# Kernel tuning notes

Measured on AMD Instinct MI355X. Metric: run time of the kernel, lower is better.

The kernel has to match this reference:

```python
import jax, jax.numpy as jnp
import numpy as np

# dims
B, N = 8, 16384
MODEL_DIM = 256
F = 32        # feature_dim
H = 4         # num_heads
G = 32        # grid_size
G3 = G * G * G
EPS = 1e-5


def setup_inputs() -> dict:
    key = jax.random.key(0)
    ks = jax.random.split(key, 9)
    eye = jnp.broadcast_to(jnp.eye(3, dtype=jnp.float32), (H, 3, 3))
    return {
        "input_tensor": jax.random.normal(ks[0], (B, MODEL_DIM, N), dtype=jnp.float32),
        "original_points": jax.random.normal(ks[1], (B, 3, N), dtype=jnp.float32),
        # Conv1d kernel_size=1, no bias -> plain (out,in) matmul weight
        "W_kv": jax.random.normal(ks[2], (H * (F + 3), MODEL_DIM), dtype=jnp.float32) * 0.02,
        # key BN affine (orig init weight=0; use small random to exercise path)
        "key_gamma": jax.random.normal(ks[3], (H * 3,), dtype=jnp.float32) * 0.1,
        "key_beta": jax.random.normal(ks[4], (H * 3,), dtype=jnp.float32) * 0.1,
        "val_gamma": 1.0 + jax.random.normal(ks[5], (H * F,), dtype=jnp.float32) * 0.1,
        "val_beta": jax.random.normal(ks[6], (H * F,), dtype=jnp.float32) * 0.1,
        # VolTransformer: per-head affine (rotation-ish matrix + translation)
        "R": eye + jax.random.normal(ks[7], (H, 3, 3), dtype=jnp.float32) * 0.05,
        "t": jax.random.normal(ks[8], (H, 3), dtype=jnp.float32) * 0.1,
    }


def _bn(x, gamma, beta):
    # training-mode BatchNorm1d over (batch, length) per channel; x: (B, C, N)
    mean = jnp.mean(x, axis=(0, 2), keepdims=True)
    var = jnp.var(x, axis=(0, 2), keepdims=True)
    xhat = (x - mean) * jax.lax.rsqrt(var + EPS)
    return xhat * gamma[None, :, None] + beta[None, :, None]


def reference(input_tensor, original_points, W_kv, key_gamma, key_beta,
              val_gamma, val_beta, R, t):
    # 1x1 conv == channel matmul: (B, H*(F+3), N)
    kv = jnp.einsum('om,bmn->bon', W_kv, input_tensor)
    keys_offset = _bn(kv[:, :H * 3], key_gamma, key_beta)          # (B, H*3, N)
    values = _bn(kv[:, H * 3:], val_gamma, val_beta)               # (B, H*F, N)

    keys_offset = keys_offset.reshape(B, H, 3, N)
    pts = original_points[:, None, :, :] + keys_offset             # (B,H,3,N)
    # per-head affine transform (VolTransformer)
    tk = jnp.einsum('hij,bhjn->bhin', R, pts) + t[None, :, :, None]
    lattice = jnp.tanh(tk)                                         # in (-1,1)

    # DifferentiablePositions: map (-1,1) -> [0, G-1], lower corner + local frac
    pos = (lattice + 1.0) * (0.5 * (G - 1))                        # (B,H,3,N)
    idx0 = jnp.clip(jnp.floor(pos), 0.0, G - 2).astype(jnp.int32)  # (B,H,3,N)
    local = pos - idx0                                             # (B,H,3,N)

    values_t = values.reshape(B, H, F, N).transpose(0, 1, 3, 2)    # (B,H,N,F)
    bh_off = (jnp.arange(B * H, dtype=jnp.int32).reshape(B, H) * G3)[:, :, None]

    out = jnp.zeros((B * H * G3, F), dtype=values.dtype)
    # trilinear splat-scatter over the 8 grid corners
    for cx in (0, 1):
        wx = local[:, :, 0] if cx else 1.0 - local[:, :, 0]
        for cy in (0, 1):
            wy = local[:, :, 1] if cy else 1.0 - local[:, :, 1]
            for cz in (0, 1):
                wz = local[:, :, 2] if cz else 1.0 - local[:, :, 2]
                w = wx * wy * wz                                    # (B,H,N)
                flat = ((idx0[:, :, 0] + cx) * G + (idx0[:, :, 1] + cy)) * G \
                       + (idx0[:, :, 2] + cz)                       # (B,H,N)
                seg = (bh_off + flat).reshape(-1)                   # (B*H*N,)
                data = (values_t * w[..., None]).reshape(-1, F)
                out = out + jax.ops.segment_sum(data, seg, num_segments=B * H * G3)

    # (B, H*F, G, G, G)
    return out.reshape(B, H, G3, F).transpose(0, 1, 3, 2).reshape(B, H * F, G, G, G)
```

## Files before the change

### kernel.cpp

```cpp
#include <hip/hip_runtime.h>
#include <hip/hip_bf16.h>
#include <cstddef>

#define Bz 8
#define Nn 16384
#define MD 256
#define Ff 32
#define Hh 4
#define Gg 32
#define G3v 32768
#define CKV 140
#define NG 32
#define NBX 31
#define NBY 31
#define NBZ 31
#define NB2 953312
#define NCH 931

using bf16x8 = __attribute__((ext_vector_type(8))) short;
using f32x16 = __attribute__((ext_vector_type(16))) float;

__device__ __forceinline__ unsigned bf16rne(float f) {
    unsigned u = __float_as_uint(f);
    return (u + 0x7fffu + ((u >> 16) & 1u)) >> 16;
}
__device__ __forceinline__ unsigned cvt2(float lo, float hi) {
    __hip_bfloat162 hb = __float22bfloat162_rn(make_float2(lo, hi));
    union { __hip_bfloat162 b; unsigned u; } c;
    c.b = hb;
    return c.u;
}

__global__ __launch_bounds__(256) void prep_w_kernel(const float* __restrict__ W,
                                                     unsigned short* __restrict__ Wbf)
{
    const int idx = blockIdx.x * 256 + threadIdx.x;
    const int e    = idx & 7;
    const int rest = idx >> 3;
    const int m    = rest % 160;
    const int kg   = rest / 160;
    const int k    = (kg << 3) + e;
    Wbf[idx] = (m < CKV) ? (unsigned short)bf16rne(W[m * MD + k]) : (unsigned short)0;
}

__global__ __launch_bounds__(256, 3) void gemm_stats_kernel(
    const float* __restrict__ X, const unsigned short* __restrict__ Wbf,
    float* __restrict__ vals, float* __restrict__ keys,
    float* __restrict__ gsum, float* __restrict__ gsq)
{
    __shared__ unsigned XlU[4096];
    __shared__ unsigned WlU[5120];
    __shared__ float red[280];

    const int bid = blockIdx.x;
    const int b   = bid >> 7;
    const int n0  = (bid & 127) << 7;
    const int t   = threadIdx.x;
    const int w   = t >> 6;
    const int ln  = t & 31;
    const int hi  = (t >> 5) & 1;

    f32x16 acc[5];
    #pragma unroll
    for (int mt = 0; mt < 5; ++mt)
        #pragma unroll
        for (int j = 0; j < 16; ++j) acc[mt][j] = 0.f;

    for (int ks = 0; ks < 4; ++ks) {
        const int k0 = ks << 6;
        if (ks > 0) __syncthreads();

        #pragma unroll
        for (int it = 0; it < 4; ++it) {
            const int a  = t + (it << 8);
            const int kp = a >> 5;
            const int n4 = (a & 31) << 2;
            const float4 r0 = *reinterpret_cast<const float4*>(
                X + (size_t)(b * MD + k0 + 2 * kp) * Nn + n0 + n4);
            const float4 r1 = *reinterpret_cast<const float4*>(
                X + (size_t)(b * MD + k0 + 2 * kp + 1) * Nn + n0 + n4);
            const int base = ((kp >> 2) << 9) + (n4 << 2) + (kp & 3);
            XlU[base]      = cvt2(r0.x, r1.x);
            XlU[base + 4]  = cvt2(r0.y, r1.y);
            XlU[base + 8]  = cvt2(r0.z, r1.z);
            XlU[base + 12] = cvt2(r0.w, r1.w);
        }
        {
            const unsigned* src = reinterpret_cast<const unsigned*>(Wbf) + ks * 5120;
            #pragma unroll
            for (int i = 0; i < 5; ++i) {
                const int d4 = (t + (i << 8)) << 2;
                *reinterpret_cast<uint4*>(&WlU[d4]) =
                    *reinterpret_cast<const uint4*>(&src[d4]);
            }
        }
        __syncthreads();

        const short* xs = reinterpret_cast<const short*>(XlU);
        const short* ws = reinterpret_cast<const short*>(WlU);
        #pragma unroll
        for (int kk = 0; kk < 4; ++kk) {
            const int grp = (kk << 1) + hi;
            const bf16x8 bf = *reinterpret_cast<const bf16x8*>(
                xs + (((grp << 7) + (w << 5) + ln) << 3));
            #pragma unroll
            for (int mt = 0; mt < 5; ++mt) {
                const bf16x8 af = *reinterpret_cast<const bf16x8*>(
                    ws + ((grp * 160 + (mt << 5) + ln) << 3));
                acc[mt] = __builtin_amdgcn_mfma_f32_32x32x16_bf16(af, bf, acc[mt], 0, 0, 0);
            }
        }
    }

    const int n = n0 + (w << 5) + ln;
    #pragma unroll
    for (int mt = 0; mt < 5; ++mt)
        #pragma unroll
        for (int reg = 0; reg < 16; ++reg) {
            const int ml = (reg & 3) + ((reg >> 2) << 3) + (hi << 2);
            const int c  = mt * 32 + ml;
            const float v = acc[mt][reg];
            if (c < 12) {
                const int hh = c / 3, kk2 = c - (c / 3) * 3;
                keys[(size_t)((b * Hh + hh) * 3 + kk2) * Nn + n] = v;
            } else if (c < CKV) {
                const int cv = c - 12;
                vals[((size_t)(b * Hh + (cv >> 5)) * Nn + n) * Ff + (cv & 31)] = v;
            }
        }

    red[t] = 0.f;
    if (t < 24) red[256 + t] = 0.f;
    __syncthreads();
    #pragma unroll
    for (int mt = 0; mt < 5; ++mt)
        #pragma unroll
        for (int reg = 0; reg < 16; ++reg) {
            if (mt == 4 && reg >= 8) continue;
            const int ml = (reg & 3) + ((reg >> 2) << 3) + (hi << 2);
            const int c  = mt * 32 + ml;
            float s = acc[mt][reg];
            float q = s * s;
            #pragma unroll
            for (int off = 1; off < 32; off <<= 1) {
                s += __shfl_xor(s, off);
                q += __shfl_xor(q, off);
            }
            if (ln == 0 && c < CKV) {
                atomicAdd(&red[c], s);
                atomicAdd(&red[140 + c], q);
            }
        }
    __syncthreads();
    if (t < CKV) {
        atomicAdd(&gsum[t], red[t]);
        atomicAdd(&gsq[t],  red[140 + t]);
    }
}

__global__ void finalize_kernel(const float* __restrict__ gsum, const float* __restrict__ gsq,
                                const float* __restrict__ kg, const float* __restrict__ kb,
                                const float* __restrict__ vg, const float* __restrict__ vb,
                                float* __restrict__ scale, float* __restrict__ shift)
{
    const int c = threadIdx.x;
    if (c < CKV) {
        const float inv = 1.f / (float)(Bz * Nn);
        const float m = gsum[c] * inv;
        const float v = fmaf(-m, m, gsq[c] * inv);
        float ga, be;
        if (c < 12) { ga = kg[c]; be = kb[c]; }
        else        { ga = vg[c - 12]; be = vb[c - 12]; }
        const float sc = ga * rsqrtf(v + 1e-5f);
        scale[c] = sc;
        shift[c] = fmaf(-m, sc, be);
    }
}

__global__ __launch_bounds__(256) void points_kernel(
    const float* __restrict__ keys, const float* __restrict__ orig,
    const float* __restrict__ Rm, const float* __restrict__ tv,
    const float* __restrict__ scale, const float* __restrict__ shift,
    float4* __restrict__ rec, int* __restrict__ cnt)
{
    const int bid = blockIdx.x;
    const int g   = bid >> 6;
    const int b   = g >> 2;
    const int h   = g & 3;
    const int t   = threadIdx.x;
    const int n   = ((bid & 63) << 8) + t;

    __shared__ float sR[9], st3[3], ksc[3], ksh[3];
    if (t < 9)       sR[t] = Rm[h * 9 + t];
    else if (t < 12) st3[t - 9] = tv[h * 3 + (t - 9)];
    else if (t < 15) { ksc[t - 12] = scale[h * 3 + (t - 12)];
                       ksh[t - 12] = shift[h * 3 + (t - 12)]; }
    __syncthreads();

    const float k0 = fmaf(keys[(size_t)(g * 3 + 0) * Nn + n], ksc[0], ksh[0]);
    const float k1 = fmaf(keys[(size_t)(g * 3 + 1) * Nn + n], ksc[1], ksh[1]);
    const float k2 = fmaf(keys[(size_t)(g * 3 + 2) * Nn + n], ksc[2], ksh[2]);
    const float p0 = orig[(size_t)(b * 3 + 0) * Nn + n] + k0;
    const float p1 = orig[(size_t)(b * 3 + 1) * Nn + n] + k1;
    const float p2 = orig[(size_t)(b * 3 + 2) * Nn + n] + k2;

    int   idx[3];
    float loc[3];
    #pragma unroll
    for (int d = 0; d < 3; ++d) {
        const float tk = fmaf(sR[d*3+0], p0, fmaf(sR[d*3+1], p1, fmaf(sR[d*3+2], p2, st3[d])));
        const float la = tanhf(tk);
        const float po = (la + 1.f) * 15.5f;
        float fi = floorf(po);
        fi = fminf(fmaxf(fi, 0.f), 30.f);
        idx[d] = (int)fi;
        loc[d] = po - fi;
    }

    const unsigned meta = (unsigned)n | ((unsigned)idx[2] << 14) |
                          ((unsigned)idx[1] << 19) | ((unsigned)idx[0] << 24);
    float4 r;
    r.x = __uint_as_float(meta);
    r.y = loc[0]; r.z = loc[1]; r.w = loc[2];
    rec[(size_t)g * Nn + n] = r;
    const int key = ((g * NBX + idx[0]) * NBY + idx[1]) * NBZ + idx[2];
    atomicAdd(&cnt[key], 1);
}

__global__ __launch_bounds__(256) void scan1_kernel(const int* __restrict__ cnt,
                                                    int* __restrict__ bsum)
{
    __shared__ int s[256];
    const int t = threadIdx.x;
    const int i = blockIdx.x * 1024 + t * 4;
    int v = 0;
    #pragma unroll
    for (int j = 0; j < 4; ++j) { const int idx = i + j; if (idx < NB2) v += cnt[idx]; }
    s[t] = v;
    __syncthreads();
    for (int off = 128; off > 0; off >>= 1) {
        if (t < off) s[t] += s[t + off];
        __syncthreads();
    }
    if (t == 0) bsum[blockIdx.x] = s[0];
}

__global__ __launch_bounds__(1024) void scan2_kernel(const int* __restrict__ bsum,
                                                     int* __restrict__ bscan)
{
    __shared__ int s[1024];
    const int t = threadIdx.x;
    const int v = (t < NCH) ? bsum[t] : 0;
    s[t] = v;
    __syncthreads();
    for (int off = 1; off < 1024; off <<= 1) {
        const int x = (t >= off) ? s[t - off] : 0;
        __syncthreads();
        s[t] += x;
        __syncthreads();
    }
    if (t < NCH) bscan[t] = s[t] - v;
}

__global__ __launch_bounds__(256) void scan3_kernel(const int* __restrict__ cnt,
                                                    const int* __restrict__ bscan,
                                                    int* __restrict__ basep,
                                                    int* __restrict__ cursor)
{
    __shared__ int s[256];
    const int t = threadIdx.x;
    const int i = blockIdx.x * 1024 + t * 4;
    int c[4], l[4];
    int sum = 0;
    #pragma unroll
    for (int j = 0; j < 4; ++j) {
        const int idx = i + j;
        c[j] = (idx < NB2) ? cnt[idx] : 0;
        l[j] = sum; sum += c[j];
    }
    s[t] = sum;
    __syncthreads();
    for (int off = 1; off < 256; off <<= 1) {
        const int x = (t >= off) ? s[t - off] : 0;
        __syncthreads();
        s[t] += x;
        __syncthreads();
    }
    const int off0 = bscan[blockIdx.x] + s[t] - sum;
    #pragma unroll
    for (int j = 0; j < 4; ++j) {
        const int idx = i + j;
        if (idx < NB2) { basep[idx] = off0 + l[j]; cursor[idx] = off0 + l[j]; }
    }
}

__global__ __launch_bounds__(256) void fill_kernel(
    const float4* __restrict__ rec, int* __restrict__ cursor,
    float4* __restrict__ binned)
{
    const int bid = blockIdx.x;
    const int g   = bid >> 6;
    const int t   = threadIdx.x;
    const int n   = ((bid & 63) << 8) + t;
    const float4 r = rec[(size_t)g * Nn + n];
    const unsigned meta = __float_as_uint(r.x);
    const int x0 = (meta >> 24) & 31;
    const int y0 = (meta >> 19) & 31;
    const int z0 = (meta >> 14) & 31;
    const int key = ((g * NBX + x0) * NBY + y0) * NBZ + z0;
    const int pos = atomicAdd(&cursor[key], 1);
    binned[pos] = r;
}

#define PROC(q, vq, WY)                                                      \
{                                                                            \
    const unsigned mq = __float_as_uint((q).x);                              \
    const int zq = (int)((mq >> 14) & 31u);                                  \
    if (zq != zcur) {                                                        \
        if (zcur >= 0) { const int zr = zcur + zc;                           \
                         tg[(zr << 5) + (f ^ zr)] += acc; }                  \
        acc = 0.f; zcur = zq;                                                \
    }                                                                        \
    const float wx = dx ? (1.f - (q).y) : (q).y;                             \
    const float wz = zc ? (q).w : (1.f - (q).w);                             \
    acc = fmaf(wx * (WY) * wz, fmaf(vq, scf, shf), acc);                     \
}

__global__ __launch_bounds__(1024) void gather_kernel(
    const float* __restrict__ vals, const float4* __restrict__ binned,
    const int* __restrict__ basep, const int* __restrict__ cnt,
    const float* __restrict__ scale, const float* __restrict__ shift,
    float* __restrict__ out)
{
    __shared__ float tile[16384];
    __shared__ float sscale[32], sshift[32];

    const int bid = blockIdx.x;
    const int g   = bid & 31;
    const int x   = (bid >> 5) & 31;
    const int yh  = bid >> 10;
    const int h   = g & 3;
    const int t   = threadIdx.x;

    {
        const float4 z4 = make_float4(0.f, 0.f, 0.f, 0.f);
        #pragma unroll
        for (int i = 0; i < 4; ++i)
            *reinterpret_cast<float4*>(&tile[(t << 2) + (i << 12)]) = z4;
    }
    if (t < 32) { sscale[t] = scale[12 + h * 32 + t]; sshift[t] = shift[12 + h * 32 + t]; }
    __syncthreads();

    const int f  = t & 31;
    const int zc = (t >> 5) & 1;
    const int w  = t >> 6;
    const int y  = (yh << 4) + w;
    const float scf = sscale[f], shf = sshift[f];
    const float* vg = vals + ((size_t)g << 19);
    float* const tg = &tile[w << 10];

    float acc = 0.f;
    int zcur = -2;

    #pragma unroll
    for (int dy = 0; dy < 2; ++dy) {
        const int y0 = y - 1 + dy;
        if ((unsigned)y0 > 30u) continue;
        #pragma unroll
        for (int dx = 0; dx < 2; ++dx) {
            const int x0 = x - 1 + dx;
            if ((unsigned)x0 > 30u) continue;
            const int kb = ((g * NBX + x0) * NBY + y0) * NBZ;
            int r       = basep[kb];
            const int e = basep[kb + 30] + cnt[kb + 30];

            for (; r + 8 <= e; r += 8) {
                const float4 q0 = binned[r];
                const float4 q1 = binned[r + 1];
                const float4 q2 = binned[r + 2];
                const float4 q3 = binned[r + 3];
                const float4 q4 = binned[r + 4];
                const float4 q5 = binned[r + 5];
                const float4 q6 = binned[r + 6];
                const float4 q7 = binned[r + 7];
                const float v0 = vg[((__float_as_uint(q0.x) & 16383u) << 5) + f];
                const float v1 = vg[((__float_as_uint(q1.x) & 16383u) << 5) + f];
                const float v2 = vg[((__float_as_uint(q2.x) & 16383u) << 5) + f];
                const float v3 = vg[((__float_as_uint(q3.x) & 16383u) << 5) + f];
                const float v4 = vg[((__float_as_uint(q4.x) & 16383u) << 5) + f];
                const float v5 = vg[((__float_as_uint(q5.x) & 16383u) << 5) + f];
                const float v6 = vg[((__float_as_uint(q6.x) & 16383u) << 5) + f];
                const float v7 = vg[((__float_as_uint(q7.x) & 16383u) << 5) + f];
                PROC(q0, v0, dy ? (1.f - q0.z) : q0.z);
                PROC(q1, v1, dy ? (1.f - q1.z) : q1.z);
                PROC(q2, v2, dy ? (1.f - q2.z) : q2.z);
                PROC(q3, v3, dy ? (1.f - q3.z) : q3.z);
                PROC(q4, v4, dy ? (1.f - q4.z) : q4.z);
                PROC(q5, v5, dy ? (1.f - q5.z) : q5.z);
                PROC(q6, v6, dy ? (1.f - q6.z) : q6.z);
                PROC(q7, v7, dy ? (1.f - q7.z) : q7.z);
            }
            for (; r + 4 <= e; r += 4) {
                const float4 q0 = binned[r];
                const float4 q1 = binned[r + 1];
                const float4 q2 = binned[r + 2];
                const float4 q3 = binned[r + 3];
                const float v0 = vg[((__float_as_uint(q0.x) & 16383u) << 5) + f];
                const float v1 = vg[((__float_as_uint(q1.x) & 16383u) << 5) + f];
                const float v2 = vg[((__float_as_uint(q2.x) & 16383u) << 5) + f];
                const float v3 = vg[((__float_as_uint(q3.x) & 16383u) << 5) + f];
                PROC(q0, v0, dy ? (1.f - q0.z) : q0.z);
                PROC(q1, v1, dy ? (1.f - q1.z) : q1.z);
                PROC(q2, v2, dy ? (1.f - q2.z) : q2.z);
                PROC(q3, v3, dy ? (1.f - q3.z) : q3.z);
            }
            for (; r < e; ++r) {
                const float4 q0 = binned[r];
                const float v0 = vg[((__float_as_uint(q0.x) & 16383u) << 5) + f];
                PROC(q0, v0, dy ? (1.f - q0.z) : q0.z);
            }
        }
    }
    if (zcur >= 0) {
        const int zr = zcur + zc;
        tg[(zr << 5) + (f ^ zr)] += acc;
    }
    __syncthreads();

    float* og = out + ((size_t)g << 20) + (x << 10) + (yh << 9);
    #pragma unroll
    for (int i = 0; i < 16; ++i) {
        const int lin = t + (i << 10);
        const int fp  = lin >> 9;
        const int s   = lin & 511;
        const int z   = s & 31;
        og[((size_t)fp << 15) + s] = tile[((s >> 5) << 10) + (z << 5) + (fp ^ z)];
    }
}

__global__ __launch_bounds__(256) void scatter_kernel(
    const float* __restrict__ vals, const float* __restrict__ keys,
    const float* __restrict__ orig, const float* __restrict__ Rm,
    const float* __restrict__ tv, const float* __restrict__ scale,
    const float* __restrict__ shift, float* __restrict__ out)
{
    const int bid   = blockIdx.x;
    const int g     = bid >> 5;
    const int chunk = bid & 31;
    const int b     = g >> 2;
    const int h     = g & 3;

    __shared__ float sc[32], sh[32], sR[9], st3[3], ksc[3], ksh[3];
    const int t = threadIdx.x;
    if (t < 32)      { sc[t] = scale[12 + h * 32 + t]; sh[t] = shift[12 + h * 32 + t]; }
    else if (t < 41) { sR[t - 32]  = Rm[h * 9 + (t - 32)]; }
    else if (t < 44) { st3[t - 41] = tv[h * 3 + (t - 41)]; }
    else if (t < 47) { ksc[t - 44] = scale[h * 3 + (t - 44)];
                       ksh[t - 44] = shift[h * 3 + (t - 44)]; }
    __syncthreads();

    float* const og = out + ((size_t)g << 20);

    #pragma unroll
    for (int pp = 0; pp < 2; ++pp) {
        const int n = (chunk << 9) + (pp << 8) + t;

        const float k0 = fmaf(keys[(size_t)(g * 3 + 0) * Nn + n], ksc[0], ksh[0]);
        const float k1 = fmaf(keys[(size_t)(g * 3 + 1) * Nn + n], ksc[1], ksh[1]);
        const float k2 = fmaf(keys[(size_t)(g * 3 + 2) * Nn + n], ksc[2], ksh[2]);
        const float p0 = orig[(size_t)(b * 3 + 0) * Nn + n] + k0;
        const float p1 = orig[(size_t)(b * 3 + 1) * Nn + n] + k1;
        const float p2 = orig[(size_t)(b * 3 + 2) * Nn + n] + k2;

        int   idx[3];
        float loc[3];
        #pragma unroll
        for (int d = 0; d < 3; ++d) {
            const float tk = fmaf(sR[d*3+0], p0, fmaf(sR[d*3+1], p1, fmaf(sR[d*3+2], p2, st3[d])));
            const float la = tanhf(tk);
            const float po = (la + 1.f) * 15.5f;
            float fi = floorf(po);
            fi = fminf(fmaxf(fi, 0.f), 30.f);
            idx[d] = (int)fi;
            loc[d] = po - fi;
        }
        const int cell = (idx[0] * Gg + idx[1]) * Gg + idx[2];

        float v[32];
        const float4* vp = reinterpret_cast<const float4*>(vals + ((size_t)g * Nn + n) * Ff);
        #pragma unroll
        for (int q = 0; q < 8; ++q) {
            const float4 xq = vp[q];
            v[4*q+0] = fmaf(xq.x, sc[4*q+0], sh[4*q+0]);
            v[4*q+1] = fmaf(xq.y, sc[4*q+1], sh[4*q+1]);
            v[4*q+2] = fmaf(xq.z, sc[4*q+2], sh[4*q+2]);
            v[4*q+3] = fmaf(xq.w, sc[4*q+3], sh[4*q+3]);
        }

        const float wx1 = loc[0], wx0 = 1.f - loc[0];
        const float wy1 = loc[1], wy0 = 1.f - loc[1];
        const float wz1 = loc[2], wz0 = 1.f - loc[2];
        const float cw[8] = { wx0*wy0*wz0, wx0*wy0*wz1, wx0*wy1*wz0, wx0*wy1*wz1,
                              wx1*wy0*wz0, wx1*wy0*wz1, wx1*wy1*wz0, wx1*wy1*wz1 };
        const int  co[8] = { 0, 1, 32, 33, 1024, 1025, 1056, 1057 };

        #pragma unroll
        for (int ff = 0; ff < 32; ++ff) {
            float* const pf = og + (size_t)ff * G3v + cell;
            const float vf = v[ff];
            #pragma unroll
            for (int c8 = 0; c8 < 8; ++c8) {
                atomicAdd(pf + co[c8], cw[c8] * vf);
            }
        }
    }
}

extern "C" void kernel_launch(void* const* d_in, const int* in_sizes, int n_in,
                              void* d_out, int out_size, void* d_ws, size_t ws_size,
                              hipStream_t stream)
{
    const float* X    = (const float*)d_in[0];
    const float* orig = (const float*)d_in[1];
    const float* W    = (const float*)d_in[2];
    const float* kg   = (const float*)d_in[3];
    const float* kb   = (const float*)d_in[4];
    const float* vg   = (const float*)d_in[5];
    const float* vb   = (const float*)d_in[6];
    const float* Rm   = (const float*)d_in[7];
    const float* tv   = (const float*)d_in[8];
    float* out = (float*)d_out;
    float* ws  = (float*)d_ws;

    float* vals  = ws;
    float* keys  = ws + 16777216;
    float* gsum  = ws + 18350080;
    float* gsq   = gsum + 140;
    float* scale = gsum + 280;
    float* shift = scale + 140;
    int*   cnt    = (int*)(ws + 18350848);
    int*   basep  = (int*)(ws + 19304160);
    int*   cursor = (int*)(ws + 20257472);
    int*   bsum   = (int*)(ws + 21210784);
    int*   bscan  = (int*)(ws + 21211808);
    float4* rec    = (float4*)(ws + 21212832);
    float4* binned = (float4*)(ws + 23309984);
    unsigned short* Wbf = (unsigned short*)(ws + 25407136);
    const size_t need_bytes = (size_t)25427616 * sizeof(float);

    hipMemsetAsync(gsum, 0, 280 * sizeof(float), stream);

    prep_w_kernel<<<160, 256, 0, stream>>>(W, Wbf);
    gemm_stats_kernel<<<1024, 256, 0, stream>>>(X, Wbf, vals, keys, gsum, gsq);
    finalize_kernel<<<1, 256, 0, stream>>>(gsum, gsq, kg, kb, vg, vb, scale, shift);

    if (ws_size >= need_bytes) {
        hipMemsetAsync(cnt, 0, (size_t)NB2 * sizeof(int), stream);
        points_kernel<<<2048, 256, 0, stream>>>(keys, orig, Rm, tv, scale, shift, rec, cnt);
        scan1_kernel<<<NCH, 256, 0, stream>>>(cnt, bsum);
        scan2_kernel<<<1, 1024, 0, stream>>>(bsum, bscan);
        scan3_kernel<<<NCH, 256, 0, stream>>>(cnt, bscan, basep, cursor);
        fill_kernel<<<2048, 256, 0, stream>>>(rec, cursor, binned);
        gather_kernel<<<2048, 1024, 0, stream>>>(vals, binned, basep, cnt, scale, shift, out);
    } else {
        hipMemsetAsync(out, 0, (size_t)out_size * sizeof(float), stream);
        scatter_kernel<<<1024, 256, 0, stream>>>(vals, keys, orig, Rm, tv, scale, shift, out);
    }
}
```

Before: 306.6 us.

## Accumulate gather splats with bf16 MFMA instead of scalar FMA runs

```diff
diff --git a/kernel.cpp b/kernel.cpp
--- a/kernel.cpp
+++ b/kernel.cpp
@@ -312,18 +312,17 @@
     binned[pos] = r;
 }
 
-#define PROC(q, vq, WY)                                                      \
+#define MKAB(qe, ridx, ae, ve)                                               \
 {                                                                            \
-    const unsigned mq = __float_as_uint((q).x);                              \
-    const int zq = (int)((mq >> 14) & 31u);                                  \
-    if (zq != zcur) {                                                        \
-        if (zcur >= 0) { const int zr = zcur + zc;                           \
-                         tg[(zr << 5) + (f ^ zr)] += acc; }                  \
-        acc = 0.f; zcur = zq;                                                \
-    }                                                                        \
-    const float wx = dx ? (1.f - (q).y) : (q).y;                             \
-    const float wz = zc ? (q).w : (1.f - (q).w);                             \
-    acc = fmaf(wx * (WY) * wz, fmaf(vq, scf, shf), acc);                     \
+    const unsigned mq = __float_as_uint((qe).x);                             \
+    const int z0 = (int)((mq >> 14) & 31u);                                  \
+    const float wx  = dx ? (1.f - (qe).y) : (qe).y;                          \
+    const float wy  = dy ? (1.f - (qe).z) : (qe).z;                          \
+    const float wxy = ((ridx) < e) ? wx * wy : 0.f;                          \
+    const float lz  = (qe).w;                                                \
+    ae = (ln == z0) ? (1.f - lz) * wxy                                       \
+                    : ((ln == z0 + 1) ? lz * wxy : 0.f);                     \
+    ve = fmaf(vg[(((size_t)(mq & 16383u)) << 5) + ln], scf, shf);            \
 }
 
 __global__ __launch_bounds__(1024) void gather_kernel(
@@ -342,25 +341,19 @@
     const int h   = g & 3;
     const int t   = threadIdx.x;
 
-    {
-        const float4 z4 = make_float4(0.f, 0.f, 0.f, 0.f);
-        #pragma unroll
-        for (int i = 0; i < 4; ++i)
-            *reinterpret_cast<float4*>(&tile[(t << 2) + (i << 12)]) = z4;
-    }
     if (t < 32) { sscale[t] = scale[12 + h * 32 + t]; sshift[t] = shift[12 + h * 32 + t]; }
     __syncthreads();
 
-    const int f  = t & 31;
-    const int zc = (t >> 5) & 1;
+    const int ln = t & 31;
+    const int hi = (t >> 5) & 1;
     const int w  = t >> 6;
     const int y  = (yh << 4) + w;
-    const float scf = sscale[f], shf = sshift[f];
+    const float scf = sscale[ln], shf = sshift[ln];
     const float* vg = vals + ((size_t)g << 19);
-    float* const tg = &tile[w << 10];
-
-    float acc = 0.f;
-    int zcur = -2;
+
+    f32x16 acc;
+    #pragma unroll
+    for (int j = 0; j < 16; ++j) acc[j] = 0.f;
 
     #pragma unroll
     for (int dy = 0; dy < 2; ++dy) {
@@ -374,56 +367,50 @@
             int r       = basep[kb];
             const int e = basep[kb + 30] + cnt[kb + 30];
 
-            for (; r + 8 <= e; r += 8) {
-                const float4 q0 = binned[r];
-                const float4 q1 = binned[r + 1];
-                const float4 q2 = binned[r + 2];
-                const float4 q3 = binned[r + 3];
-                const float4 q4 = binned[r + 4];
-                const float4 q5 = binned[r + 5];
-                const float4 q6 = binned[r + 6];
-                const float4 q7 = binned[r + 7];
-                const float v0 = vg[((__float_as_uint(q0.x) & 16383u) << 5) + f];
-                const float v1 = vg[((__float_as_uint(q1.x) & 16383u) << 5) + f];
-                const float v2 = vg[((__float_as_uint(q2.x) & 16383u) << 5) + f];
-                const float v3 = vg[((__float_as_uint(q3.x) & 16383u) << 5) + f];
-                const float v4 = vg[((__float_as_uint(q4.x) & 16383u) << 5) + f];
-                const float v5 = vg[((__float_as_uint(q5.x) & 16383u) << 5) + f];
-                const float v6 = vg[((__float_as_uint(q6.x) & 16383u) << 5) + f];
-                const float v7 = vg[((__float_as_uint(q7.x) & 16383u) << 5) + f];
-                PROC(q0, v0, dy ? (1.f - q0.z) : q0.z);
-                PROC(q1, v1, dy ? (1.f - q1.z) : q1.z);
-                PROC(q2, v2, dy ? (1.f - q2.z) : q2.z);
-                PROC(q3, v3, dy ? (1.f - q3.z) : q3.z);
-                PROC(q4, v4, dy ? (1.f - q4.z) : q4.z);
-                PROC(q5, v5, dy ? (1.f - q5.z) : q5.z);
-                PROC(q6, v6, dy ? (1.f - q6.z) : q6.z);
-                PROC(q7, v7, dy ? (1.f - q7.z) : q7.z);
-            }
-            for (; r + 4 <= e; r += 4) {
-                const float4 q0 = binned[r];
-                const float4 q1 = binned[r + 1];
-                const float4 q2 = binned[r + 2];
-                const float4 q3 = binned[r + 3];
-                const float v0 = vg[((__float_as_uint(q0.x) & 16383u) << 5) + f];
-                const float v1 = vg[((__float_as_uint(q1.x) & 16383u) << 5) + f];
-                const float v2 = vg[((__float_as_uint(q2.x) & 16383u) << 5) + f];
-                const float v3 = vg[((__float_as_uint(q3.x) & 16383u) << 5) + f];
-                PROC(q0, v0, dy ? (1.f - q0.z) : q0.z);
-                PROC(q1, v1, dy ? (1.f - q1.z) : q1.z);
-                PROC(q2, v2, dy ? (1.f - q2.z) : q2.z);
-                PROC(q3, v3, dy ? (1.f - q3.z) : q3.z);
-            }
-            for (; r < e; ++r) {
-                const float4 q0 = binned[r];
-                const float v0 = vg[((__float_as_uint(q0.x) & 16383u) << 5) + f];
-                PROC(q0, v0, dy ? (1.f - q0.z) : q0.z);
-            }
-        }
-    }
-    if (zcur >= 0) {
-        const int zr = zcur + zc;
-        tg[(zr << 5) + (f ^ zr)] += acc;
+            for (; r < e; r += 16) {
+                const int base = r + (hi << 3);
+                const int eM1  = e - 1;
+                const int r0 = min(base,     eM1);
+                const int r1 = min(base + 1, eM1);
+                const int r2 = min(base + 2, eM1);
+                const int r3 = min(base + 3, eM1);
+                const int r4 = min(base + 4, eM1);
+                const int r5 = min(base + 5, eM1);
+                const int r6 = min(base + 6, eM1);
+                const int r7 = min(base + 7, eM1);
+                const float4 q0 = binned[r0];
+                const float4 q1 = binned[r1];
+                const float4 q2 = binned[r2];
+                const float4 q3 = binned[r3];
+                const float4 q4 = binned[r4];
+                const float4 q5 = binned[r5];
+                const float4 q6 = binned[r6];
+                const float4 q7 = binned[r7];
+                float a0, a1, a2, a3, a4, a5, a6, a7;
+                float v0, v1, v2, v3, v4, v5, v6, v7;
+                MKAB(q0, base,     a0, v0);
+                MKAB(q1, base + 1, a1, v1);
+                MKAB(q2, base + 2, a2, v2);
+                MKAB(q3, base + 3, a3, v3);
+                MKAB(q4, base + 4, a4, v4);
+                MKAB(q5, base + 5, a5, v5);
+                MKAB(q6, base + 6, a6, v6);
+                MKAB(q7, base + 7, a7, v7);
+                union { bf16x8 v; unsigned u[4]; } af, bf;
+                af.u[0] = cvt2(a0, a1); af.u[1] = cvt2(a2, a3);
+                af.u[2] = cvt2(a4, a5); af.u[3] = cvt2(a6, a7);
+                bf.u[0] = cvt2(v0, v1); bf.u[1] = cvt2(v2, v3);
+                bf.u[2] = cvt2(v4, v5); bf.u[3] = cvt2(v6, v7);
+                acc = __builtin_amdgcn_mfma_f32_32x32x16_bf16(af.v, bf.v, acc, 0, 0, 0);
+            }
+        }
+    }
+
+    float* const tg = &tile[w << 10];
+    #pragma unroll
+    for (int reg = 0; reg < 16; ++reg) {
+        const int zr = (reg & 3) + ((reg >> 2) << 3) + (hi << 2);
+        tg[(zr << 5) + ((ln ^ zr) & 31)] = acc[reg];
     }
     __syncthreads();
 
@@ -434,7 +421,7 @@
         const int fp  = lin >> 9;
         const int s   = lin & 511;
         const int z   = s & 31;
-        og[((size_t)fp << 15) + s] = tile[((s >> 5) << 10) + (z << 5) + (fp ^ z)];
+        og[((size_t)fp << 15) + s] = tile[((s >> 5) << 10) + (z << 5) + ((fp ^ z) & 31)];
     }
 }
 
```

Measured after the change: 291.8 us. 4.8% less time.
